# Performance work log

Measured on AMD Instinct MI355X. Metric: run time of the kernel, lower is better.

Reference implementation:

```python
import jax, jax.numpy as jnp
import numpy as np
from jax import lax

B, C, L = 2048, 9605, 8
WL_PER_LABEL = 50
ALPHA = 0.5        # training_config['alpha4']
ALPHA1 = 0.1       # margin
ALPHA2 = 2.0       # training_config['alpha2']
ALPHA3 = 10.0      # training_config['alpha3']
ALPHA_OTHER = 0.5
NEG = jnp.float32(-1e30)


def setup_inputs() -> dict:
    key = jax.random.key(0)
    k1, k2, k3, k4 = jax.random.split(key, 4)
    x = jax.random.normal(k1, (B, C), dtype=jnp.float32) * 2.0
    y = (jax.random.uniform(k2, (B, C)) < 0.005).astype(jnp.float32)
    y_neg = (jax.random.uniform(k3, (B, C)) < 0.005).astype(jnp.float32)
    # whitelist masks: L app-labels, each whitelisting ~WL_PER_LABEL raw classes
    idx = jax.random.randint(k4, (L, WL_PER_LABEL), 0, C)
    wl_masks = jnp.zeros((L, C), dtype=bool).at[jnp.arange(L)[:, None], idx].set(True)
    return {"x": x, "y": y, "y_neg": y_neg, "wl_masks": wl_masks}


def reference(x, y, y_neg, wl_masks):
    # y_neg is consumed by the original forward (find_gt_whitelist) but never
    # affects the returned loss, faithfully ignored here.
    xs_pos = jax.nn.sigmoid(x)                                  # [B, C]
    # top_k_thres = max(11th-largest sigmoid, alpha_other)
    thres = jnp.maximum(lax.top_k(xs_pos, 11)[0][:, 10], ALPHA_OTHER)  # [B]
    # per-label whitelist max: m[b,l] = max_{c in wl_l} xs_pos[b,c]
    m = jnp.max(jnp.where(wl_masks[None, :, :], xs_pos[:, None, :], NEG), axis=-1)  # [B, L]
    # label l is a ground-truth whitelist label iff y has any positive in wl_l
    has_pos = jnp.einsum('bc,lc->bl', y, wl_masks.astype(y.dtype)) > 0   # [B, L]
    correct_max = jnp.max(jnp.where(has_pos, m, NEG), axis=-1)           # [B]
    incorrect_max = jnp.max(jnp.where(~has_pos, m, NEG), axis=-1)        # [B]
    any_correct = jnp.any(has_pos, axis=-1)
    any_incorrect = jnp.any(~has_pos, axis=-1)
    # union whitelist max (the "other" branch uses xs_pos over all wl indices)
    union_max = jnp.max(jnp.where(jnp.any(wl_masks, axis=0)[None, :], xs_pos, NEG), axis=-1)
    x1 = jnp.where(any_correct, correct_max, thres)
    x2 = jnp.where(any_correct,
                   jnp.where(any_incorrect, jnp.maximum(incorrect_max, thres), thres),
                   union_max)
    coef = jnp.where(any_correct, 1.0, 1.0 - ALPHA)
    d = x2 - x1 + ALPHA1
    rank = jnp.where(d > 0, ALPHA2, 1.0) * jax.nn.sigmoid(ALPHA3 * d)
    return jnp.mean(coef * rank)
```

## Files before the change

### kernel.cpp

```cpp
#include <hip/hip_runtime.h>

#define CC 9605
#define BB 2048
#define LL 8
#define CAND_MAX 384
#define NEGF (-1e30f)
#define NINF (-__builtin_huge_valf())
#define LOMIN 0x00800000u

#define WS_PARTIALS_OFF 16384
#define WS_ROWMAX_OFF 24576

__device__ __forceinline__ unsigned enc_f(float f) {
  unsigned u = __float_as_uint(f);
  return (u & 0x80000000u) ? ~u : (u | 0x80000000u);
}
__device__ __forceinline__ float dec_u(unsigned e) {
  unsigned u = (e & 0x80000000u) ? (e & 0x7fffffffu) : ~e;
  return __uint_as_float(u);
}
__device__ __forceinline__ float sigm(float z) {
  return 1.0f / (1.0f + __expf(-z));
}

__global__ void wl_sniff(const unsigned* __restrict__ wlw,
                         unsigned* __restrict__ wsu) {
  const int nwords = (LL * CC) / 4;
  const int stride = gridDim.x * blockDim.x;
  unsigned f = 0u;
  for (int j = blockIdx.x * blockDim.x + threadIdx.x; j < nwords; j += stride) {
    unsigned w = wlw[j];
#pragma unroll
    for (int k = 0; k < 4; ++k) {
      unsigned b = (w >> (8 * k)) & 255u;
      if (b == 1u)    { f |= 2u; if (k != 0) f |= 1u; }
      if (b == 0x3fu) { f |= 8u; if (k == 1) f |= 4u; }
    }
  }
#pragma unroll
  for (int off = 32; off >= 1; off >>= 1) f |= __shfl_xor(f, off, 64);
  if ((threadIdx.x & 63) == 0 && f) atomicOr(&wsu[1], f);
}

__global__ void wl_compact(const unsigned char* __restrict__ wl,
                           unsigned* __restrict__ wsu) {
  const int tid = threadIdx.x;
  const int lane = tid & 63;
  const int c = blockIdx.x * 256 + tid;
  const unsigned g = wsu[1];
  const int dt = (g & 1u) ? 0 : (g & 4u) ? 3 : (g & 2u) ? 1 : (g & 8u) ? 2 : 0;
  const int* wl32 = (const int*)wl;
  const float* wlf = (const float*)wl;
  const unsigned short* wlh = (const unsigned short*)wl;
  unsigned m = 0u;
  if (c < CC) {
#pragma unroll
    for (int l = 0; l < LL; ++l) {
      int j = l * CC + c;
      bool on;
      if (dt == 0) on = (wl[j] != 0);
      else if (dt == 1) on = (wl32[j] != 0);
      else if (dt == 2) on = (wlf[j] != 0.0f);
      else on = (wlh[j] != 0);
      if (on) m |= (1u << l);
    }
  }
  unsigned long long bal = __ballot(m != 0u);
  if (bal) {
    unsigned wcnt = (unsigned)__popcll(bal);
    unsigned basep = 0u;
    if (lane == 0) basep = atomicAdd(&wsu[0], wcnt);
    basep = __shfl(basep, 0, 64);
    if (m) {
      unsigned pos = basep + (unsigned)__popcll(bal & ((1ull << lane) - 1ull));
      if (pos < 2048u) wsu[4 + pos] = ((unsigned)c << 8) | m;
    }
  }
}

__global__ __launch_bounds__(256) void rowmax_kernel(
    const float* __restrict__ x, unsigned* __restrict__ rowmax) {
  __shared__ float shm[4];
  const int tid = threadIdx.x, lane = tid & 63, wid = tid >> 6;
  const int r = blockIdx.x;
  const long long base = (long long)r * CC;
  const int soff = (4 - (r & 3)) & 3;
  const int ng = (CC - soff) >> 2;
  const int tailn = CC - soff - (ng << 2);
  const int m_extra = soff + tailn;
  const float4* vp = (const float4*)(x + base + soff);
  float m = NINF;
#pragma unroll
  for (int k = 0; k < 9; ++k) {
    float4 t = vp[tid + (k << 8)];
    m = fmaxf(m, fmaxf(fmaxf(t.x, t.y), fmaxf(t.z, t.w)));
  }
  {
    int gi = tid + 2304;
    if (gi < ng) {
      float4 t = vp[gi];
      m = fmaxf(m, fmaxf(fmaxf(t.x, t.y), fmaxf(t.z, t.w)));
    }
  }
  if (tid < m_extra) {
    int tc = (tid < soff) ? tid : (soff + (ng << 2) + (tid - soff));
    m = fmaxf(m, x[base + tc]);
  }
#pragma unroll
  for (int off = 32; off >= 1; off >>= 1) m = fmaxf(m, __shfl_xor(m, off, 64));
  if (lane == 0) shm[wid] = m;
  __syncthreads();
  if (tid == 0)
    rowmax[r] = enc_f(fmaxf(fmaxf(shm[0], shm[1]), fmaxf(shm[2], shm[3])));
}


#define FOR8(OP) OP(0) OP(1) OP(2) OP(3) OP(4) OP(5) OP(6) OP(7)

#define APPEND1(V, PRED)                                                     \
  {                                                                          \
    bool _p = (PRED);                                                        \
    unsigned long long _bal = __ballot(_p);                                  \
    if (_bal) {                                                              \
      unsigned _wt = (unsigned)__popcll(_bal);                               \
      unsigned _bp = 0u;                                                     \
      if (lane == 0) _bp = atomicAdd(&sh_cnt, _wt);                          \
      _bp = __shfl(_bp, 0, 64);                                              \
      if (_p) {                                                              \
        unsigned _pos =                                                      \
            _bp + (unsigned)__popcll(_bal & ((1ull << lane) - 1ull));        \
        if (_pos < CAND_MAX) sh_cand[_pos] = enc_f(V);                       \
      }                                                                      \
    }                                                                        \
  }

#define COMPACT_PASS(TENC, RES)                                              \
  do {                                                                       \
    float Tf = dec_u(TENC);                                                  \
    __syncthreads();                                                         \
    if (tid == 0) sh_cnt = 0u;                                               \
    __syncthreads();                                                         \
    _Pragma("unroll") for (int k = 0; k < 9; ++k) {                          \
      float4 t = vp[tid + (k << 8)];                                         \
      APPEND1(t.x, t.x >= Tf) APPEND1(t.y, t.y >= Tf)                        \
      APPEND1(t.z, t.z >= Tf) APPEND1(t.w, t.w >= Tf)                        \
    }                                                                        \
    {                                                                        \
      float4 t = make_float4(NINF, NINF, NINF, NINF);                        \
      if (tid + 2304 < ng) t = vp[tid + 2304];                               \
      APPEND1(t.x, t.x >= Tf) APPEND1(t.y, t.y >= Tf)                        \
      APPEND1(t.z, t.z >= Tf) APPEND1(t.w, t.w >= Tf)                        \
    }                                                                        \
    APPEND1(tailv, tailv >= Tf)                                              \
    __syncthreads();                                                         \
    RES = sh_cnt;                                                            \
  } while (0)

#define COUNT_PASS(TENC, RES)                                                \
  do {                                                                       \
    float Tf = dec_u(TENC);                                                  \
    unsigned cl = 0u;                                                        \
    _Pragma("unroll") for (int k = 0; k < 9; ++k) {                          \
      float4 t = vp[tid + (k << 8)];                                         \
      cl += (t.x >= Tf) + (t.y >= Tf) + (t.z >= Tf) + (t.w >= Tf);           \
    }                                                                        \
    {                                                                        \
      float4 t = make_float4(NINF, NINF, NINF, NINF);                        \
      if (tid + 2304 < ng) t = vp[tid + 2304];                               \
      cl += (t.x >= Tf) + (t.y >= Tf) + (t.z >= Tf) + (t.w >= Tf);           \
    }                                                                        \
    cl += (tailv >= Tf) ? 1u : 0u;                                           \
    _Pragma("unroll") for (int off = 32; off >= 1; off >>= 1)                \
        cl += __shfl_xor(cl, off, 64);                                       \
    __syncthreads();                                                         \
    if (lane == 0) sh_redC[wid] = cl;                                        \
    __syncthreads();                                                         \
    RES = sh_redC[0] + sh_redC[1] + sh_redC[2] + sh_redC[3];                 \
  } while (0)

__global__ __launch_bounds__(256) void loss_kernel(
    const float* __restrict__ x, const float* __restrict__ y,
    const unsigned* __restrict__ wsu, const unsigned* __restrict__ rowmax,
    float* __restrict__ partials) {
  __shared__ unsigned sh_cand[CAND_MAX];
  __shared__ unsigned sh_redC[4];
  __shared__ unsigned sh_cnt;
  __shared__ float sh_wlm[4][8];
  __shared__ unsigned sh_wpm[4];

  const int tid = threadIdx.x, lane = tid & 63, wid = tid >> 6;
  const int r = blockIdx.x;
  const long long base = (long long)r * CC;
  const int soff = (4 - (r & 3)) & 3;
  const int ng = (CC - soff) >> 2;
  const int tailn = CC - soff - (ng << 2);
  const int m_extra = soff + tailn;
  const float4* vp = (const float4*)(x + base + soff);
  float tailv = NINF;
  if (tid < m_extra) {
    int tc = (tid < soff) ? tid : (soff + (ng << 2) + (tid - soff));
    tailv = x[base + tc];
  }
  const unsigned Emax = rowmax[r];
  const unsigned nu = min(wsu[0], 2048u);
  const unsigned* ents = wsu + 4;

  unsigned lo = (Emax > LOMIN + (1u << 22)) ? Emax - (1u << 22) : LOMIN;
  unsigned hi = Emax + 1u;
  unsigned c;
  bool done = false;
  unsigned E11 = 0u;
  COMPACT_PASS(lo, c);
  unsigned compLo = lo;
  while (c < 11u && lo > LOMIN) {
    hi = lo;
    lo = (lo > LOMIN + (1u << 23)) ? lo - (1u << 23) : LOMIN;
    COMPACT_PASS(lo, c);
    compLo = lo;
  }
  if (c < 11u) { E11 = LOMIN; done = true; }
  while (!done && c > CAND_MAX) {
    if (hi - lo <= 1u) { E11 = lo; done = true; break; }
    unsigned mid = lo + ((hi - lo) >> 1);
    unsigned cm;
    COUNT_PASS(mid, cm);
    if (cm >= 11u) { lo = mid; c = cm; } else { hi = mid; }
  }
  if (!done && lo != compLo) { COMPACT_PASS(lo, c); }

  unsigned en0 = ((unsigned)tid < nu) ? ents[tid] : 0u;
  unsigned en1 = ((unsigned)tid + 256u < nu) ? ents[tid + 256] : 0u;
  float gx0 = x[base + (en0 >> 8)], gy0 = y[base + (en0 >> 8)];
  float gx1 = x[base + (en1 >> 8)], gy1 = y[base + (en1 >> 8)];
#define DECL_LM(k) float lm_##k = NEGF;
  FOR8(DECL_LM)
  unsigned pmask = 0u;
#define FOLDE(EN, GX, GY)                                        \
  {                                                              \
    unsigned mk = (EN) & 255u;                                   \
    pmask |= mk;                                                 \
    if ((GY) > 0.0f) pmask |= (mk << 8);                         \
    if (mk & 1u)   lm_0 = fmaxf(lm_0, (GX));                     \
    if (mk & 2u)   lm_1 = fmaxf(lm_1, (GX));                     \
    if (mk & 4u)   lm_2 = fmaxf(lm_2, (GX));                     \
    if (mk & 8u)   lm_3 = fmaxf(lm_3, (GX));                     \
    if (mk & 16u)  lm_4 = fmaxf(lm_4, (GX));                     \
    if (mk & 32u)  lm_5 = fmaxf(lm_5, (GX));                     \
    if (mk & 64u)  lm_6 = fmaxf(lm_6, (GX));                     \
    if (mk & 128u) lm_7 = fmaxf(lm_7, (GX));                     \
  }
  FOLDE(en0, gx0, gy0)
  FOLDE(en1, gx1, gy1)
  for (unsigned e = 512u + (unsigned)tid; e < nu; e += 256u) {
    unsigned ent = ents[e];
    float xv = x[base + (ent >> 8)];
    float yv = y[base + (ent >> 8)];
    FOLDE(ent, xv, yv)
  }
#pragma unroll
  for (int off = 32; off >= 1; off >>= 1) {
    pmask |= __shfl_xor(pmask, off, 64);
#define RED1(l) lm_##l = fmaxf(lm_##l, __shfl_xor(lm_##l, off, 64));
    FOR8(RED1)
#undef RED1
  }
  if (lane == 0) {
#define STL(l) sh_wlm[wid][l] = lm_##l;
    FOR8(STL)
#undef STL
    sh_wpm[wid] = pmask;
  }
  __syncthreads();
  if (wid != 0) return;

  if (!done) {
    unsigned c0 = ((unsigned)lane < c) ? sh_cand[lane] : 0u;
    unsigned c1 = ((unsigned)lane + 64u < c) ? sh_cand[lane + 64u] : 0u;
    unsigned c2 = ((unsigned)lane + 128u < c) ? sh_cand[lane + 128u] : 0u;
    unsigned c3 = ((unsigned)lane + 192u < c) ? sh_cand[lane + 192u] : 0u;
    unsigned c4 = ((unsigned)lane + 256u < c) ? sh_cand[lane + 256u] : 0u;
    unsigned c5 = ((unsigned)lane + 320u < c) ? sh_cand[lane + 320u] : 0u;
    unsigned blo = lo, bhi = hi;
    while (bhi - blo > 1u) {
      unsigned mid = blo + ((bhi - blo) >> 1);
      unsigned cnt = (unsigned)__popcll(__ballot(c0 >= mid)) +
                     (unsigned)__popcll(__ballot(c1 >= mid)) +
                     (unsigned)__popcll(__ballot(c2 >= mid)) +
                     (unsigned)__popcll(__ballot(c3 >= mid)) +
                     (unsigned)__popcll(__ballot(c4 >= mid)) +
                     (unsigned)__popcll(__ballot(c5 >= mid));
      if (cnt >= 11u) blo = mid; else bhi = mid;
    }
    E11 = blo;
  }

  if (lane == 0) {
#pragma unroll
    for (int j = 1; j < 4; ++j) {
      pmask |= sh_wpm[j];
#define CMB(l) lm_##l = fmaxf(lm_##l, sh_wlm[j][l]);
      FOR8(CMB)
#undef CMB
    }
    unsigned PR = pmask & 255u, PO = (pmask >> 8) & 255u;
    float thres = fmaxf(sigm(dec_u(E11)), 0.5f);
    float cmax = NEGF, imax = NEGF, umax = NEGF;
#define EP1(l)                                                   \
    if ((PR >> l) & 1u) {                                        \
      float ml = sigm(lm_##l);                                   \
      umax = fmaxf(umax, ml);                                    \
      if ((PO >> l) & 1u) cmax = fmaxf(cmax, ml);                \
      else imax = fmaxf(imax, ml);                               \
    }
    FOR8(EP1)
#undef EP1
    bool anyc = (PO != 0u);
    bool anyi = (PO != 255u);
    float x1 = anyc ? cmax : thres;
    float x2 = anyc ? (anyi ? fmaxf(imax, thres) : thres)
                    : ((nu > 0u) ? umax : NEGF);
    float coef = anyc ? 1.0f : 0.5f;
    float dd = x2 - x1 + 0.1f;
    float rank = ((dd > 0.0f) ? 2.0f : 1.0f) * sigm(10.0f * dd);
    partials[r] = coef * rank;
  }
}

__global__ void final_reduce(const float* __restrict__ partials,
                             float* __restrict__ out) {
  __shared__ float sh[4];
  const int tid = threadIdx.x;
  const int lane = tid & 63;
  const int wid = tid >> 6;
  float s = 0.0f;
  for (int i = tid; i < BB; i += 256) s += partials[i];
#pragma unroll
  for (int off = 32; off >= 1; off >>= 1) s += __shfl_xor(s, off, 64);
  if (lane == 0) sh[wid] = s;
  __syncthreads();
  if (tid == 0) out[0] = (sh[0] + sh[1] + sh[2] + sh[3]) * (1.0f / (float)BB);
}

extern "C" void kernel_launch(void* const* d_in, const int* in_sizes, int n_in,
                              void* d_out, int out_size, void* d_ws,
                              size_t ws_size, hipStream_t stream) {
  const float* x = (const float*)d_in[0];
  const float* y = (const float*)d_in[1];
  const unsigned char* wl = (const unsigned char*)d_in[3];
  float* out = (float*)d_out;
  unsigned* wsu = (unsigned*)d_ws;
  float* partials = (float*)((char*)d_ws + WS_PARTIALS_OFF);
  unsigned* rowmax = (unsigned*)((char*)d_ws + WS_ROWMAX_OFF);

  hipMemsetAsync(d_ws, 0, 16, stream);
  wl_sniff<<<64, 256, 0, stream>>>((const unsigned*)wl, wsu);
  wl_compact<<<(CC + 255) / 256, 256, 0, stream>>>(wl, wsu);
  rowmax_kernel<<<BB, 256, 0, stream>>>(x, rowmax);
  loss_kernel<<<BB, 256, 0, stream>>>(x, y, wsu, rowmax, partials);
  final_reduce<<<1, 256, 0, stream>>>(partials, out);
}
```

Before: 248.1 us.

## Fuse rowmax into loss kernel and select top-11 via per-thread-max candidate pruning

Drops the separate rowmax kernel. Each thread now computes its own strided maximum and keeps it in shared memory. Wave 0 finds the 11th-largest per-thread max, which is a lower bound on the 11th-largest element. Only the threads whose max clears that bound are revisited to gather candidates, and a wave-local ballot append replaces the shared atomic counter. This removes one full pass over x and several block-wide barrier passes, but the candidate gather and refinement now run serially on a single wave per row.

```diff
diff --git a/kernel.cpp b/kernel.cpp
--- a/kernel.cpp
+++ b/kernel.cpp
@@ -9,7 +9,6 @@
 #define LOMIN 0x00800000u
 
 #define WS_PARTIALS_OFF 16384
-#define WS_ROWMAX_OFF 24576
 
 __device__ __forceinline__ unsigned enc_f(float f) {
   unsigned u = __float_as_uint(f);
@@ -78,9 +77,30 @@
   }
 }
 
-__global__ __launch_bounds__(256) void rowmax_kernel(
-    const float* __restrict__ x, unsigned* __restrict__ rowmax) {
-  __shared__ float shm[4];
+
+#define FOR8(OP) OP(0) OP(1) OP(2) OP(3) OP(4) OP(5) OP(6) OP(7)
+
+#define WAPPEND(V, P)                                                        \
+  {                                                                          \
+    bool _p = (P);                                                           \
+    unsigned long long _bal = __ballot(_p);                                  \
+    if (_p) {                                                                \
+      unsigned _pos =                                                        \
+          cnt + (unsigned)__popcll(_bal & ((1ull << lane) - 1ull));          \
+      if (_pos < CAND_MAX) sh_cand[_pos] = enc_f(V);                         \
+    }                                                                        \
+    cnt += (unsigned)__popcll(_bal);                                         \
+  }
+
+__global__ __launch_bounds__(256) void loss_kernel(
+    const float* __restrict__ x, const float* __restrict__ y,
+    const unsigned* __restrict__ wsu, float* __restrict__ partials) {
+  __shared__ float sh_pm[256];
+  __shared__ unsigned sh_list[256];
+  __shared__ unsigned sh_cand[CAND_MAX];
+  __shared__ float sh_wlm[4][8];
+  __shared__ unsigned sh_wpm[4];
+
   const int tid = threadIdx.x, lane = tid & 63, wid = tid >> 6;
   const int r = blockIdx.x;
   const long long base = (long long)r * CC;
@@ -89,6 +109,7 @@
   const int tailn = CC - soff - (ng << 2);
   const int m_extra = soff + tailn;
   const float4* vp = (const float4*)(x + base + soff);
+
   float m = NINF;
 #pragma unroll
   for (int k = 0; k < 9; ++k) {
@@ -106,128 +127,10 @@
     int tc = (tid < soff) ? tid : (soff + (ng << 2) + (tid - soff));
     m = fmaxf(m, x[base + tc]);
   }
-#pragma unroll
-  for (int off = 32; off >= 1; off >>= 1) m = fmaxf(m, __shfl_xor(m, off, 64));
-  if (lane == 0) shm[wid] = m;
-  __syncthreads();
-  if (tid == 0)
-    rowmax[r] = enc_f(fmaxf(fmaxf(shm[0], shm[1]), fmaxf(shm[2], shm[3])));
-}
-
-
-#define FOR8(OP) OP(0) OP(1) OP(2) OP(3) OP(4) OP(5) OP(6) OP(7)
-
-#define APPEND1(V, PRED)                                                     \
-  {                                                                          \
-    bool _p = (PRED);                                                        \
-    unsigned long long _bal = __ballot(_p);                                  \
-    if (_bal) {                                                              \
-      unsigned _wt = (unsigned)__popcll(_bal);                               \
-      unsigned _bp = 0u;                                                     \
-      if (lane == 0) _bp = atomicAdd(&sh_cnt, _wt);                          \
-      _bp = __shfl(_bp, 0, 64);                                              \
-      if (_p) {                                                              \
-        unsigned _pos =                                                      \
-            _bp + (unsigned)__popcll(_bal & ((1ull << lane) - 1ull));        \
-        if (_pos < CAND_MAX) sh_cand[_pos] = enc_f(V);                       \
-      }                                                                      \
-    }                                                                        \
-  }
-
-#define COMPACT_PASS(TENC, RES)                                              \
-  do {                                                                       \
-    float Tf = dec_u(TENC);                                                  \
-    __syncthreads();                                                         \
-    if (tid == 0) sh_cnt = 0u;                                               \
-    __syncthreads();                                                         \
-    _Pragma("unroll") for (int k = 0; k < 9; ++k) {                          \
-      float4 t = vp[tid + (k << 8)];                                         \
-      APPEND1(t.x, t.x >= Tf) APPEND1(t.y, t.y >= Tf)                        \
-      APPEND1(t.z, t.z >= Tf) APPEND1(t.w, t.w >= Tf)                        \
-    }                                                                        \
-    {                                                                        \
-      float4 t = make_float4(NINF, NINF, NINF, NINF);                        \
-      if (tid + 2304 < ng) t = vp[tid + 2304];                               \
-      APPEND1(t.x, t.x >= Tf) APPEND1(t.y, t.y >= Tf)                        \
-      APPEND1(t.z, t.z >= Tf) APPEND1(t.w, t.w >= Tf)                        \
-    }                                                                        \
-    APPEND1(tailv, tailv >= Tf)                                              \
-    __syncthreads();                                                         \
-    RES = sh_cnt;                                                            \
-  } while (0)
-
-#define COUNT_PASS(TENC, RES)                                                \
-  do {                                                                       \
-    float Tf = dec_u(TENC);                                                  \
-    unsigned cl = 0u;                                                        \
-    _Pragma("unroll") for (int k = 0; k < 9; ++k) {                          \
-      float4 t = vp[tid + (k << 8)];                                         \
-      cl += (t.x >= Tf) + (t.y >= Tf) + (t.z >= Tf) + (t.w >= Tf);           \
-    }                                                                        \
-    {                                                                        \
-      float4 t = make_float4(NINF, NINF, NINF, NINF);                        \
-      if (tid + 2304 < ng) t = vp[tid + 2304];                               \
-      cl += (t.x >= Tf) + (t.y >= Tf) + (t.z >= Tf) + (t.w >= Tf);           \
-    }                                                                        \
-    cl += (tailv >= Tf) ? 1u : 0u;                                           \
-    _Pragma("unroll") for (int off = 32; off >= 1; off >>= 1)                \
-        cl += __shfl_xor(cl, off, 64);                                       \
-    __syncthreads();                                                         \
-    if (lane == 0) sh_redC[wid] = cl;                                        \
-    __syncthreads();                                                         \
-    RES = sh_redC[0] + sh_redC[1] + sh_redC[2] + sh_redC[3];                 \
-  } while (0)
-
-__global__ __launch_bounds__(256) void loss_kernel(
-    const float* __restrict__ x, const float* __restrict__ y,
-    const unsigned* __restrict__ wsu, const unsigned* __restrict__ rowmax,
-    float* __restrict__ partials) {
-  __shared__ unsigned sh_cand[CAND_MAX];
-  __shared__ unsigned sh_redC[4];
-  __shared__ unsigned sh_cnt;
-  __shared__ float sh_wlm[4][8];
-  __shared__ unsigned sh_wpm[4];
-
-  const int tid = threadIdx.x, lane = tid & 63, wid = tid >> 6;
-  const int r = blockIdx.x;
-  const long long base = (long long)r * CC;
-  const int soff = (4 - (r & 3)) & 3;
-  const int ng = (CC - soff) >> 2;
-  const int tailn = CC - soff - (ng << 2);
-  const int m_extra = soff + tailn;
-  const float4* vp = (const float4*)(x + base + soff);
-  float tailv = NINF;
-  if (tid < m_extra) {
-    int tc = (tid < soff) ? tid : (soff + (ng << 2) + (tid - soff));
-    tailv = x[base + tc];
-  }
-  const unsigned Emax = rowmax[r];
+  sh_pm[tid] = m;
+
   const unsigned nu = min(wsu[0], 2048u);
   const unsigned* ents = wsu + 4;
-
-  unsigned lo = (Emax > LOMIN + (1u << 22)) ? Emax - (1u << 22) : LOMIN;
-  unsigned hi = Emax + 1u;
-  unsigned c;
-  bool done = false;
-  unsigned E11 = 0u;
-  COMPACT_PASS(lo, c);
-  unsigned compLo = lo;
-  while (c < 11u && lo > LOMIN) {
-    hi = lo;
-    lo = (lo > LOMIN + (1u << 23)) ? lo - (1u << 23) : LOMIN;
-    COMPACT_PASS(lo, c);
-    compLo = lo;
-  }
-  if (c < 11u) { E11 = LOMIN; done = true; }
-  while (!done && c > CAND_MAX) {
-    if (hi - lo <= 1u) { E11 = lo; done = true; break; }
-    unsigned mid = lo + ((hi - lo) >> 1);
-    unsigned cm;
-    COUNT_PASS(mid, cm);
-    if (cm >= 11u) { lo = mid; c = cm; } else { hi = mid; }
-  }
-  if (!done && lo != compLo) { COMPACT_PASS(lo, c); }
-
   unsigned en0 = ((unsigned)tid < nu) ? ents[tid] : 0u;
   unsigned en1 = ((unsigned)tid + 256u < nu) ? ents[tid + 256] : 0u;
   float gx0 = x[base + (en0 >> 8)], gy0 = y[base + (en0 >> 8)];
@@ -270,26 +173,126 @@
 #undef STL
     sh_wpm[wid] = pmask;
   }
+
   __syncthreads();
   if (wid != 0) return;
 
+  unsigned ep0 = enc_f(sh_pm[lane]);
+  unsigned ep1 = enc_f(sh_pm[lane + 64]);
+  unsigned ep2 = enc_f(sh_pm[lane + 128]);
+  unsigned ep3 = enc_f(sh_pm[lane + 192]);
+  unsigned eEmax = max(max(ep0, ep1), max(ep2, ep3));
+#pragma unroll
+  for (int off = 32; off >= 1; off >>= 1)
+    eEmax = max(eEmax, __shfl_xor(eEmax, off, 64));
+  unsigned lo = min(LOMIN, eEmax), hi = eEmax + 1u;
+  while (hi - lo > 1u) {
+    unsigned mid = lo + ((hi - lo) >> 1);
+    unsigned c4 = ((ep0 >= mid) ? 1u : 0u) + ((ep1 >= mid) ? 1u : 0u) +
+                  ((ep2 >= mid) ? 1u : 0u) + ((ep3 >= mid) ? 1u : 0u);
+    unsigned tot = (unsigned)__popcll(__ballot(c4 & 1u)) +
+                   ((unsigned)__popcll(__ballot(c4 & 2u)) << 1) +
+                   ((unsigned)__popcll(__ballot(c4 & 4u)) << 2);
+    if (tot >= 11u) lo = mid; else hi = mid;
+  }
+  const unsigned ecm11 = lo;
+  hi = eEmax + 1u;
+
+  unsigned ncc = 0u;
+#define LISTJ(EP, J)                                                         \
+  {                                                                          \
+    bool _p = ((EP) >= ecm11);                                               \
+    unsigned long long _bal = __ballot(_p);                                  \
+    if (_p) sh_list[ncc + (unsigned)__popcll(_bal & ((1ull << lane) - 1ull))] \
+        = (unsigned)(lane + 64 * (J));                                       \
+    ncc += (unsigned)__popcll(_bal);                                         \
+  }
+  LISTJ(ep0, 0) LISTJ(ep1, 1) LISTJ(ep2, 2) LISTJ(ep3, 3)
+#undef LISTJ
+
+#define CAND_COMPACT(TENC, RES)                                              \
+  do {                                                                       \
+    float Tf = dec_u(TENC);                                                  \
+    unsigned cnt = 0u;                                                       \
+    for (unsigned i0 = 0; i0 < ncc; i0 += 64u) {           \
+      unsigned i = i0 + (unsigned)lane;                                      \
+      bool have = (i < ncc);                                                 \
+      int cch = have ? (int)sh_list[i] : 0;                                  \
+      for (int j = 0; j < 10; ++j) {                                         \
+        bool ok = have && ((j < 9) || (cch + 2304 < ng));                    \
+        float4 t = make_float4(NINF, NINF, NINF, NINF);                      \
+        if (ok) t = vp[cch + (j << 8)];                                      \
+        WAPPEND(t.x, t.x >= Tf) WAPPEND(t.y, t.y >= Tf)                      \
+        WAPPEND(t.z, t.z >= Tf) WAPPEND(t.w, t.w >= Tf)                      \
+      }                                                                      \
+      float tv = NINF;                                                       \
+      if (have && cch < m_extra) {                                           \
+        int tc = (cch < soff) ? cch : (soff + (ng << 2) + (cch - soff));     \
+        tv = x[base + tc];                                                   \
+      }                                                                      \
+      WAPPEND(tv, tv >= Tf)                                                  \
+    }                                                                        \
+    RES = cnt;                                                               \
+  } while (0)
+
+#define CAND_COUNT(TENC, RES)                                                \
+  do {                                                                       \
+    float Tf = dec_u(TENC);                                                  \
+    unsigned cl = 0u;                                                        \
+    for (unsigned i0 = 0; i0 < ncc; i0 += 64u) {                             \
+      unsigned i = i0 + (unsigned)lane;                                      \
+      bool have = (i < ncc);                                                 \
+      int cch = have ? (int)sh_list[i] : 0;                                  \
+      for (int j = 0; j < 10; ++j) {                                         \
+        bool ok = have && ((j < 9) || (cch + 2304 < ng));                    \
+        float4 t = make_float4(NINF, NINF, NINF, NINF);                      \
+        if (ok) t = vp[cch + (j << 8)];                                      \
+        cl += (t.x >= Tf) + (t.y >= Tf) + (t.z >= Tf) + (t.w >= Tf);         \
+      }                                                                      \
+      float tv = NINF;                                                       \
+      if (have && cch < m_extra) {                                           \
+        int tc = (cch < soff) ? cch : (soff + (ng << 2) + (cch - soff));     \
+        tv = x[base + tc];                                                   \
+      }                                                                      \
+      cl += (tv >= Tf) ? 1u : 0u;                                            \
+    }                                                                        \
+    _Pragma("unroll") for (int off = 32; off >= 1; off >>= 1)                \
+        cl += __shfl_xor(cl, off, 64);                                       \
+    RES = cl;                                                                \
+  } while (0)
+
+  unsigned c;
+  CAND_COMPACT(lo, c);
+  unsigned compT = lo;
+  unsigned E11 = lo;
+  bool done = false;
+  if (c < 11u) done = true;
+  while (!done && c > CAND_MAX) {
+    if (hi - lo <= 1u) { E11 = lo; done = true; break; }
+    unsigned mid = lo + ((hi - lo) >> 1);
+    unsigned cm;
+    CAND_COUNT(mid, cm);
+    if (cm >= 11u) { lo = mid; c = cm; } else { hi = mid; }
+  }
+  if (!done && lo != compT) { CAND_COMPACT(lo, c); }
+
   if (!done) {
-    unsigned c0 = ((unsigned)lane < c) ? sh_cand[lane] : 0u;
-    unsigned c1 = ((unsigned)lane + 64u < c) ? sh_cand[lane + 64u] : 0u;
-    unsigned c2 = ((unsigned)lane + 128u < c) ? sh_cand[lane + 128u] : 0u;
-    unsigned c3 = ((unsigned)lane + 192u < c) ? sh_cand[lane + 192u] : 0u;
-    unsigned c4 = ((unsigned)lane + 256u < c) ? sh_cand[lane + 256u] : 0u;
-    unsigned c5 = ((unsigned)lane + 320u < c) ? sh_cand[lane + 320u] : 0u;
+    unsigned cc0 = ((unsigned)lane < c) ? sh_cand[lane] : 0u;
+    unsigned cc1 = ((unsigned)lane + 64u < c) ? sh_cand[lane + 64u] : 0u;
+    unsigned cc2 = ((unsigned)lane + 128u < c) ? sh_cand[lane + 128u] : 0u;
+    unsigned cc3 = ((unsigned)lane + 192u < c) ? sh_cand[lane + 192u] : 0u;
+    unsigned cc4 = ((unsigned)lane + 256u < c) ? sh_cand[lane + 256u] : 0u;
+    unsigned cc5 = ((unsigned)lane + 320u < c) ? sh_cand[lane + 320u] : 0u;
     unsigned blo = lo, bhi = hi;
     while (bhi - blo > 1u) {
       unsigned mid = blo + ((bhi - blo) >> 1);
-      unsigned cnt = (unsigned)__popcll(__ballot(c0 >= mid)) +
-                     (unsigned)__popcll(__ballot(c1 >= mid)) +
-                     (unsigned)__popcll(__ballot(c2 >= mid)) +
-                     (unsigned)__popcll(__ballot(c3 >= mid)) +
-                     (unsigned)__popcll(__ballot(c4 >= mid)) +
-                     (unsigned)__popcll(__ballot(c5 >= mid));
-      if (cnt >= 11u) blo = mid; else bhi = mid;
+      unsigned cnt2 = (unsigned)__popcll(__ballot(cc0 >= mid)) +
+                      (unsigned)__popcll(__ballot(cc1 >= mid)) +
+                      (unsigned)__popcll(__ballot(cc2 >= mid)) +
+                      (unsigned)__popcll(__ballot(cc3 >= mid)) +
+                      (unsigned)__popcll(__ballot(cc4 >= mid)) +
+                      (unsigned)__popcll(__ballot(cc5 >= mid));
+      if (cnt2 >= 11u) blo = mid; else bhi = mid;
     }
     E11 = blo;
   }
@@ -350,12 +353,10 @@
   float* out = (float*)d_out;
   unsigned* wsu = (unsigned*)d_ws;
   float* partials = (float*)((char*)d_ws + WS_PARTIALS_OFF);
-  unsigned* rowmax = (unsigned*)((char*)d_ws + WS_ROWMAX_OFF);
 
   hipMemsetAsync(d_ws, 0, 16, stream);
   wl_sniff<<<64, 256, 0, stream>>>((const unsigned*)wl, wsu);
   wl_compact<<<(CC + 255) / 256, 256, 0, stream>>>(wl, wsu);
-  rowmax_kernel<<<BB, 256, 0, stream>>>(x, rowmax);
-  loss_kernel<<<BB, 256, 0, stream>>>(x, y, wsu, rowmax, partials);
+  loss_kernel<<<BB, 256, 0, stream>>>(x, y, wsu, partials);
   final_reduce<<<1, 256, 0, stream>>>(partials, out);
 }
```

After: 228.8 us. -7.8%, faster.
